# Kernel tuning notes

Hardware: AMD Instinct MI355X
Metric: run time of the kernel (lower is better)

Reference implementation:

```python
import jax, jax.numpy as jnp
import numpy as np
from jax import lax

NUM_ITER = 20


def setup_inputs() -> dict:
    key = jax.random.key(0)
    k1, k2, k3, k4 = jax.random.split(key, 4)
    B, C, H, W = 4, 16, 384, 384
    z_k = jax.random.normal(k1, (B, 2, H, W), dtype=jnp.float32)
    x0 = jax.random.normal(k2, (B, 2, H, W), dtype=jnp.float32)
    csm = jax.random.normal(k3, (B, 2, C, H, W), dtype=jnp.float32)
    mask = jax.random.randint(k4, (B, H, W), 0, 2, dtype=jnp.int32)
    lam = jnp.asarray([0.05], dtype=jnp.float32)  # nn.Parameter init value
    return {"z_k": z_k, "x0": x0, "csm": csm, "lam": lam, "mask": mask}


def _r2c(x):
    # [.., 2, ...] real at axis 1 -> complex
    return lax.complex(x[:, 0], x[:, 1])


def reference(z_k, x0, csm, lam, mask):
    zc = _r2c(z_k)          # [B,H,W] complex64
    b = _r2c(x0)            # [B,H,W] complex64
    coil = _r2c(csm)        # [B,C,H,W] complex64
    m = mask.astype(jnp.float32)  # [B,H,W] binary sampling mask
    lam_s = lam[0]

    def A_fwd(x):           # image [B,H,W] -> masked coil k-space [B,C,H,W]
        return m[:, None] * jnp.fft.fft2(coil * x[:, None])

    def A_adj(k):           # coil k-space [B,C,H,W] -> image [B,H,W]
        return jnp.sum(jnp.conj(coil) * jnp.fft.ifft2(m[:, None] * k), axis=1)

    L = 1.0

    def body(i, carry):
        x, y, t = carry
        grad = A_adj(A_fwd(y) - b[:, None])
        xn = y - (1.0 / L) * grad
        xn = xn - lam_s * (xn - zc)
        # complex prox: clamp real and imag parts at 0
        xn = lax.complex(jnp.maximum(xn.real, 0.0), jnp.maximum(xn.imag, 0.0))
        tn = (1.0 + jnp.sqrt(1.0 + 4.0 * t * t)) / 2.0
        yn = xn + (t - 1.0) / tn * (xn - x)
        return xn, yn, tn

    x_init = jnp.zeros_like(b)
    x, y, t = lax.fori_loop(0, NUM_ITER, body,
                            (x_init, x_init, jnp.float32(1.0)))
    # c2r along axis=1
    return jnp.stack([x.real, x.imag], axis=1)
```

## Files before the change

kernel.cpp:

```cpp
#include <hip/hip_runtime.h>
#include <math.h>


#define NN 384
#define BB 4
#define CC 16
#define NITER 20
#define LNPAD 432
#define PI_F 3.14159265358979323846f
#define TWOPI_F 6.28318530717958647692f

__device__ __forceinline__ int LID(int i) { return i + (i >> 3); }

__device__ __forceinline__ float2 cmulf(float2 a, float2 b) {
  return make_float2(a.x * b.x - a.y * b.y, a.x * b.y + a.y * b.x);
}

template<int CTRL>
__device__ __forceinline__ float dppx(float v) {
  int s = __float_as_int(v);
  return __int_as_float(__builtin_amdgcn_update_dpp(s, s, CTRL, 0xF, 0xF, true));
}

template<int H>
__device__ __forceinline__ float2 exch(float2 v) {
  if constexpr (H == 1) {
    return make_float2(dppx<0xB1>(v.x), dppx<0xB1>(v.y));
  } else if constexpr (H == 2) {
    return make_float2(dppx<0x4E>(v.x), dppx<0x4E>(v.y));
  } else if constexpr (H == 8) {
    return make_float2(dppx<0x128>(v.x), dppx<0x128>(v.y));
  } else {
    return make_float2(__shfl_xor(v.x, H), __shfl_xor(v.y, H));
  }
}

template<int DIR>
__device__ __forceinline__ void dft4(float2* v) {
  float ax = v[0].x + v[2].x, ay = v[0].y + v[2].y;
  float bx = v[0].x - v[2].x, by = v[0].y - v[2].y;
  float cx = v[1].x + v[3].x, cy = v[1].y + v[3].y;
  float dx = v[1].x - v[3].x, dy = v[1].y - v[3].y;
  float dix, diy;
  if (DIR < 0) { dix = dy; diy = -dx; }
  else         { dix = -dy; diy = dx; }
  v[0] = make_float2(ax + cx, ay + cy);
  v[2] = make_float2(ax - cx, ay - cy);
  v[1] = make_float2(bx + dix, by + diy);
  v[3] = make_float2(bx - dix, by - diy);
}

template<int SIGN>
__device__ __forceinline__ void dft3(float2 a, float2 b, float2 c,
                                     float2& X0, float2& X1, float2& X2) {
  const float S3 = 0.86602540378443864676f;
  float ux = b.x + c.x, uy = b.y + c.y;
  float dx = b.x - c.x, dy = b.y - c.y;
  float mx = a.x - 0.5f * ux, my = a.y - 0.5f * uy;
  float ex = S3 * dx, ey = S3 * dy;
  X0 = make_float2(a.x + ux, a.y + uy);
  if (SIGN < 0) {
    X1 = make_float2(mx + ey, my - ex);
    X2 = make_float2(mx - ey, my + ex);
  } else {
    X1 = make_float2(mx - ey, my + ex);
    X2 = make_float2(mx + ey, my - ex);
  }
}

template<int SIGN>
__device__ __forceinline__ void dft6(float2* v) {
  const float S3 = 0.86602540378443864676f;
  float2 E0, E1, E2, O0, O1, O2;
  dft3<SIGN>(v[0], v[2], v[4], E0, E1, E2);
  dft3<SIGN>(v[1], v[3], v[5], O0, O1, O2);
  const float ss = (SIGN < 0) ? -S3 : S3;
  float2 T1 = cmulf(O1, make_float2(0.5f, ss));
  float2 T2 = cmulf(O2, make_float2(-0.5f, ss));
  v[0] = make_float2(E0.x + O0.x, E0.y + O0.y);
  v[1] = make_float2(E1.x + T1.x, E1.y + T1.y);
  v[2] = make_float2(E2.x + T2.x, E2.y + T2.y);
  v[3] = make_float2(E0.x - O0.x, E0.y - O0.y);
  v[4] = make_float2(E1.x - T1.x, E1.y - T1.y);
  v[5] = make_float2(E2.x - T2.x, E2.y - T2.y);
}


template<int H>
__device__ __forceinline__ void dif_step1(float2 v[6], float s, float csl, float snl) {
#pragma unroll
  for (int r = 0; r < 6; ++r) {
    float2 o = exch<H>(v[r]);
    float dx = fmaf(s, v[r].x, o.x);
    float dy = fmaf(s, v[r].y, o.y);
    v[r] = make_float2(dx * csl - dy * snl, dx * snl + dy * csl);
  }
}
template<int H>
__device__ __forceinline__ void dif_step1_notw(float2 v[6], float s) {
#pragma unroll
  for (int r = 0; r < 6; ++r) {
    float2 o = exch<H>(v[r]);
    v[r] = make_float2(fmaf(s, v[r].x, o.x), fmaf(s, v[r].y, o.y));
  }
}
template<int H>
__device__ __forceinline__ void dif_step2(float2 u[6], float2 v[6],
                                          float s, float csl, float snl) {
#pragma unroll
  for (int r = 0; r < 6; ++r) {
    float2 ou = exch<H>(u[r]);
    float2 ov = exch<H>(v[r]);
    float dux = fmaf(s, u[r].x, ou.x), duy = fmaf(s, u[r].y, ou.y);
    float dvx = fmaf(s, v[r].x, ov.x), dvy = fmaf(s, v[r].y, ov.y);
    u[r] = make_float2(dux * csl - duy * snl, dux * snl + duy * csl);
    v[r] = make_float2(dvx * csl - dvy * snl, dvx * snl + dvy * csl);
  }
}
template<int H>
__device__ __forceinline__ void dif_step2_notw(float2 u[6], float2 v[6], float s) {
#pragma unroll
  for (int r = 0; r < 6; ++r) {
    float2 ou = exch<H>(u[r]);
    float2 ov = exch<H>(v[r]);
    u[r] = make_float2(fmaf(s, u[r].x, ou.x), fmaf(s, u[r].y, ou.y));
    v[r] = make_float2(fmaf(s, v[r].x, ov.x), fmaf(s, v[r].y, ov.y));
  }
}

template<int H>
__device__ __forceinline__ void dit_step2(float2 u[6], float2 v[6],
                                          float s, float csl, float snl) {
#pragma unroll
  for (int r = 0; r < 6; ++r) {
    float2 bu = make_float2(u[r].x * csl - u[r].y * snl, u[r].x * snl + u[r].y * csl);
    float2 bv = make_float2(v[r].x * csl - v[r].y * snl, v[r].x * snl + v[r].y * csl);
    float2 ou = exch<H>(bu);
    float2 ov = exch<H>(bv);
    u[r] = make_float2(fmaf(s, bu.x, ou.x), fmaf(s, bu.y, ou.y));
    v[r] = make_float2(fmaf(s, bv.x, ov.x), fmaf(s, bv.y, ov.y));
  }
}
template<int H>
__device__ __forceinline__ void dit_step2_notw(float2 u[6], float2 v[6], float s) {
#pragma unroll
  for (int r = 0; r < 6; ++r) {
    float2 ou = exch<H>(u[r]);
    float2 ov = exch<H>(v[r]);
    u[r] = make_float2(fmaf(s, u[r].x, ou.x), fmaf(s, u[r].y, ou.y));
    v[r] = make_float2(fmaf(s, v[r].x, ov.x), fmaf(s, v[r].y, ov.y));
  }
}

template<int SIGN>
__device__ __forceinline__ void dif64t(float2 v[6], int t, float tc, float tss) {
  { int j = t & 31; bool hi = (t & 32) != 0;
    float cs = __shfl(tc, j), sn = __shfl(tss, j);
    float s = hi ? -1.f : 1.f, csl = hi ? cs : 1.f, snl = hi ? sn : 0.f;
    dif_step1<32>(v, s, csl, snl); }
  { int j = (t & 15) << 1; bool hi = (t & 16) != 0;
    float cs = __shfl(tc, j), sn = __shfl(tss, j);
    float s = hi ? -1.f : 1.f, csl = hi ? cs : 1.f, snl = hi ? sn : 0.f;
    dif_step1<16>(v, s, csl, snl); }
  { int j = (t & 7) << 2; bool hi = (t & 8) != 0;
    float cs = __shfl(tc, j), sn = __shfl(tss, j);
    float s = hi ? -1.f : 1.f, csl = hi ? cs : 1.f, snl = hi ? sn : 0.f;
    dif_step1<8>(v, s, csl, snl); }
  { int j = (t & 3) << 3; bool hi = (t & 4) != 0;
    float cs = __shfl(tc, j), sn = __shfl(tss, j);
    float s = hi ? -1.f : 1.f, csl = hi ? cs : 1.f, snl = hi ? sn : 0.f;
    dif_step1<4>(v, s, csl, snl); }
  { bool hi = (t & 2) != 0, iq = (t & 1) != 0;
    float s = hi ? -1.f : 1.f;
    float c2 = (hi && iq) ? 0.f : 1.f;
    float s2 = (hi && iq) ? (float)SIGN : 0.f;
    dif_step1<2>(v, s, c2, s2); }
  { bool hi = (t & 1) != 0;
    float s = hi ? -1.f : 1.f;
    dif_step1_notw<1>(v, s); }
}

template<int SIGN>
__device__ __forceinline__ void dif64t2(float2 u[6], float2 v[6], int t,
                                        float tc, float tss) {
  { int j = t & 31; bool hi = (t & 32) != 0;
    float cs = __shfl(tc, j), sn = __shfl(tss, j);
    float s = hi ? -1.f : 1.f, csl = hi ? cs : 1.f, snl = hi ? sn : 0.f;
    dif_step2<32>(u, v, s, csl, snl); }
  { int j = (t & 15) << 1; bool hi = (t & 16) != 0;
    float cs = __shfl(tc, j), sn = __shfl(tss, j);
    float s = hi ? -1.f : 1.f, csl = hi ? cs : 1.f, snl = hi ? sn : 0.f;
    dif_step2<16>(u, v, s, csl, snl); }
  { int j = (t & 7) << 2; bool hi = (t & 8) != 0;
    float cs = __shfl(tc, j), sn = __shfl(tss, j);
    float s = hi ? -1.f : 1.f, csl = hi ? cs : 1.f, snl = hi ? sn : 0.f;
    dif_step2<8>(u, v, s, csl, snl); }
  { int j = (t & 3) << 3; bool hi = (t & 4) != 0;
    float cs = __shfl(tc, j), sn = __shfl(tss, j);
    float s = hi ? -1.f : 1.f, csl = hi ? cs : 1.f, snl = hi ? sn : 0.f;
    dif_step2<4>(u, v, s, csl, snl); }
  { bool hi = (t & 2) != 0, iq = (t & 1) != 0;
    float s = hi ? -1.f : 1.f;
    float c2 = (hi && iq) ? 0.f : 1.f;
    float s2 = (hi && iq) ? (float)SIGN : 0.f;
    dif_step2<2>(u, v, s, c2, s2); }
  { bool hi = (t & 1) != 0;
    float s = hi ? -1.f : 1.f;
    dif_step2_notw<1>(u, v, s); }
}

template<int SIGN>
__device__ __forceinline__ void dit64t2(float2 u[6], float2 v[6], int t,
                                        float tc, float tss) {
  { bool hi = (t & 1) != 0;
    float s = hi ? -1.f : 1.f;
    dit_step2_notw<1>(u, v, s); }
  { bool hi = (t & 2) != 0, iq = (t & 1) != 0;
    float s = hi ? -1.f : 1.f;
    float c2 = (hi && iq) ? 0.f : 1.f;
    float s2 = (hi && iq) ? (float)SIGN : 0.f;
    dit_step2<2>(u, v, s, c2, s2); }
  { int j = (t & 3) << 3; bool hi = (t & 4) != 0;
    float cs = __shfl(tc, j), sn = __shfl(tss, j);
    float s = hi ? -1.f : 1.f, csl = hi ? cs : 1.f, snl = hi ? sn : 0.f;
    dit_step2<4>(u, v, s, csl, snl); }
  { int j = (t & 7) << 2; bool hi = (t & 8) != 0;
    float cs = __shfl(tc, j), sn = __shfl(tss, j);
    float s = hi ? -1.f : 1.f, csl = hi ? cs : 1.f, snl = hi ? sn : 0.f;
    dit_step2<8>(u, v, s, csl, snl); }
  { int j = (t & 15) << 1; bool hi = (t & 16) != 0;
    float cs = __shfl(tc, j), sn = __shfl(tss, j);
    float s = hi ? -1.f : 1.f, csl = hi ? cs : 1.f, snl = hi ? sn : 0.f;
    dit_step2<16>(u, v, s, csl, snl); }
  { int j = t & 31; bool hi = (t & 32) != 0;
    float cs = __shfl(tc, j), sn = __shfl(tss, j);
    float s = hi ? -1.f : 1.f, csl = hi ? cs : 1.f, snl = hi ? sn : 0.f;
    dit_step2<32>(u, v, s, csl, snl); }
}

template<int SIGN>
__device__ __forceinline__ void fwd384t(float2 v[6], int t, float tc, float tss,
                                        const float2 w[5]) {
  dft6<SIGN>(v);
#pragma unroll
  for (int r = 1; r < 6; ++r) v[r] = cmulf(v[r], w[r - 1]);
  dif64t<SIGN>(v, t, tc, tss);
}

template<int SIGN>
__device__ __forceinline__ void fwd384t2(float2 u[6], float2 v[6], int t,
                                         float tc, float tss, const float2 w[5]) {
  dft6<SIGN>(u);
  dft6<SIGN>(v);
#pragma unroll
  for (int r = 1; r < 6; ++r) { u[r] = cmulf(u[r], w[r - 1]); v[r] = cmulf(v[r], w[r - 1]); }
  dif64t2<SIGN>(u, v, t, tc, tss);
}

template<int SIGN>
__device__ __forceinline__ void bwd384t2(float2 u[6], float2 v[6], int t,
                                         float tc, float tss, const float2 w[5],
                                         float sc0) {
  dit64t2<SIGN>(u, v, t, tc, tss);
  u[0].x *= sc0; u[0].y *= sc0;
  v[0].x *= sc0; v[0].y *= sc0;
#pragma unroll
  for (int r = 1; r < 6; ++r) { u[r] = cmulf(u[r], w[r - 1]); v[r] = cmulf(v[r], w[r - 1]); }
  dft6<SIGN>(u);
  dft6<SIGN>(v);
}

template<int R, int NS, int DIR>
__device__ __forceinline__ void fft_stage(const float2* S, float2* D, int t) {
  constexpr int NR = NN / R;
#pragma unroll
  for (int rep = 0; rep < (NR + 63) / 64; ++rep) {
    int j = t + rep * 64;
    if (j < NR) {
      float2 v[R];
#pragma unroll
      for (int r = 0; r < R; ++r) v[r] = S[LID(j + r * NR)];
      if constexpr (NS > 1) {
        float ang = (float)DIR * (TWOPI_F / (float)(NS * R)) * (float)(j % NS);
        float sv, cv;
        __sincosf(ang, &sv, &cv);
        float2 w = make_float2(cv, sv);
        float2 wr = w;
#pragma unroll
        for (int r = 1; r < R; ++r) { v[r] = cmulf(v[r], wr); wr = cmulf(wr, w); }
      }
      if constexpr (R == 4) dft4<DIR>(v); else dft6<DIR>(v);
      int base = (j / NS) * (NS * R) + (j % NS);
#pragma unroll
      for (int r = 0; r < R; ++r) D[LID(base + r * NS)] = v[r];
    }
  }
}

template<int DIR>
__device__ __forceinline__ void fft384(float2* A, float2* Bf, int t) {
  fft_stage<4, 1,  DIR>(A,  Bf, t); __syncthreads();
  fft_stage<4, 4,  DIR>(Bf, A,  t); __syncthreads();
  fft_stage<4, 16, DIR>(A,  Bf, t); __syncthreads();
  fft_stage<6, 64, DIR>(Bf, A,  t); __syncthreads();
}

__global__ __launch_bounds__(256) void k_e(const float2* __restrict__ czb,
                                           float2* __restrict__ xbuf,
                                           float2* __restrict__ ybuf) {
  long i = (long)blockIdx.x * 256 + threadIdx.x;
  float2 cz = czb[i];
  float2 x = make_float2(fmaxf(cz.x, 0.f), fmaxf(cz.y, 0.f));
  xbuf[i] = x;
  ybuf[i] = x;
}

__global__ __launch_bounds__(256) void k_p1(const float2* __restrict__ ybuf,
                                            const float* __restrict__ csm,
                                            float2* __restrict__ W1) {
  int t = threadIdx.x & 63;
  int w = threadIdx.x >> 6;
  long gl = (long)blockIdx.x * 4 + w;
  int y = (int)(gl % NN);
  long bc = gl / NN;
  long b = bc >> 4, c = bc & 15;
  long rowoff = (long)y * NN;
  float tc, ts; __sincosf((float)(t & 31) * (PI_F / 32.0f), &ts, &tc);
  float tsf = -ts;
  float2 w0; __sincosf(-(float)t * (TWOPI_F / 384.0f), &w0.y, &w0.x);
  float2 wf[5];
  wf[0] = w0;
#pragma unroll
  for (int r = 1; r < 5; ++r) wf[r] = cmulf(wf[r - 1], w0);
  const float2* yrow = ybuf + b * (long)(NN * NN) + rowoff;
  const float* crow_re = csm + (b * 2 * CC + c) * (long)(NN * NN) + rowoff;
  const float* crow_im = crow_re + (long)CC * NN * NN;
  float2 v[6];
#pragma unroll
  for (int k = 0; k < 6; ++k) {
    int x = t + 64 * k;
    float2 yv = yrow[x];
    float cre = crow_re[x], cim = crow_im[x];
    v[k] = make_float2(yv.x * cre - yv.y * cim, yv.x * cim + yv.y * cre);
  }
  fwd384t<-1>(v, t, tc, tsf, wf);
  float2* orow = W1 + gl * NN;
#pragma unroll
  for (int r = 0; r < 6; ++r) orow[t + 64 * r] = v[r];
}

#define P2PAD 392
__global__ __launch_bounds__(256) void k_p2(float2* __restrict__ W1,
                                            const unsigned char* __restrict__ maskPT) {
  __shared__ float ldsR[8][P2PAD];
  __shared__ float ldsI[8][P2PAD];
  int tid = threadIdx.x;
  const int nwg = BB * CC * (NN / 8);
  int l = ((int)blockIdx.x & 7) * (nwg >> 3) + ((int)blockIdx.x >> 3);
  int xt = l % (NN / 8);
  long bc = l / (NN / 8);
  long b = bc >> 4;
  int s0 = xt * 8;
  long sbase = bc * (long)(NN * NN);
  int w = tid >> 6, t = tid & 63;
  float tc, ts; __sincosf((float)(t & 31) * (PI_F / 32.0f), &ts, &tc);
  float tsf = -ts;
  float2 w0; __sincosf(-(float)t * (TWOPI_F / 384.0f), &w0.y, &w0.x);
  float2 wf[5], wb[5];
  wf[0] = w0;
#pragma unroll
  for (int r = 1; r < 5; ++r) wf[r] = cmulf(wf[r - 1], w0);
  const float inv = 1.0f / NN;
#pragma unroll
  for (int r = 0; r < 5; ++r) wb[r] = make_float2(wf[r].x * inv, -wf[r].y * inv);
  const float4* W1v = (const float4*)W1;
  long f4base = (sbase >> 1) + (s0 >> 1);
#pragma unroll
  for (int k = 0; k < 6; ++k) {
    int e = tid + k * 256; int y = e >> 2; int q = e & 3;
    float4 val = W1v[f4base + (long)y * (NN / 2) + q];
    ldsR[2 * q][y] = val.x; ldsI[2 * q][y] = val.y;
    ldsR[2 * q + 1][y] = val.z; ldsI[2 * q + 1][y] = val.w;
  }
  __syncthreads();
  const unsigned char* mb = maskPT + b * (long)(NN * NN);
  {
    int c0 = 2 * w, c1 = 2 * w + 1;
    float2 u[6], v[6];
#pragma unroll
    for (int k = 0; k < 6; ++k) {
      u[k] = make_float2(ldsR[c0][t + 64 * k], ldsI[c0][t + 64 * k]);
      v[k] = make_float2(ldsR[c1][t + 64 * k], ldsI[c1][t + 64 * k]);
    }
    fwd384t2<-1>(u, v, t, tc, tsf, wf);
    const unsigned char* m0 = mb + (long)(s0 + c0) * NN;
    const unsigned char* m1 = mb + (long)(s0 + c1) * NN;
#pragma unroll
    for (int r = 0; r < 6; ++r) {
      float mv0 = (float)m0[t + 64 * r];
      float mv1 = (float)m1[t + 64 * r];
      u[r].x *= mv0; u[r].y *= mv0;
      v[r].x *= mv1; v[r].y *= mv1;
    }
    bwd384t2<1>(u, v, t, tc, ts, wb, inv);
#pragma unroll
    for (int k = 0; k < 6; ++k) {
      ldsR[c0][t + 64 * k] = u[k].x;
      ldsI[c0][t + 64 * k] = u[k].y;
      ldsR[c1][t + 64 * k] = v[k].x;
      ldsI[c1][t + 64 * k] = v[k].y;
    }
  }
  __syncthreads();
  float4* W1o = (float4*)W1;
#pragma unroll
  for (int k = 0; k < 6; ++k) {
    int e = tid + k * 256; int y = e >> 2; int q = e & 3;
    float4 val;
    val.x = ldsR[2 * q][y]; val.y = ldsI[2 * q][y];
    val.z = ldsR[2 * q + 1][y]; val.w = ldsI[2 * q + 1][y];
    W1o[f4base + (long)y * (NN / 2) + q] = val;
  }
}

__global__ __launch_bounds__(256) void k_p3(const float2* __restrict__ W1,
                                            const float* __restrict__ csm,
                                            const float2* __restrict__ czb,
                                            const float* __restrict__ lamp,
                                            float2* __restrict__ xbuf,
                                            float2* __restrict__ ybuf,
                                            float* __restrict__ outp,
                                            float beta, int last) {
  __shared__ float2 part[4][NN];
  int tid = threadIdx.x;
  int w = tid >> 6, t = tid & 63;
  long gl = blockIdx.x;
  long b = gl / NN;
  int y = (int)(gl % NN);
  long rowoff = (long)y * NN;
  float tc, ts; __sincosf((float)(t & 31) * (PI_F / 32.0f), &ts, &tc);
  float2 w0; __sincosf((float)t * (TWOPI_F / 384.0f), &w0.y, &w0.x);
  float2 wb[5];
  wb[0] = w0;
#pragma unroll
  for (int r = 1; r < 5; ++r) wb[r] = cmulf(wb[r - 1], w0);
  float2 acc[6];
#pragma unroll
  for (int k = 0; k < 6; ++k) acc[k] = make_float2(0.f, 0.f);
#pragma unroll
  for (int ci = 0; ci < 4; ci += 2) {
    int c0 = w * 4 + ci, c1 = c0 + 1;
    const float2* row0 = W1 + ((b * CC + c0) * (long)NN + y) * NN;
    const float2* row1 = W1 + ((b * CC + c1) * (long)NN + y) * NN;
    float2 u[6], v[6];
#pragma unroll
    for (int r = 0; r < 6; ++r) { u[r] = row0[t + 64 * r]; v[r] = row1[t + 64 * r]; }
    bwd384t2<1>(u, v, t, tc, ts, wb, 1.0f);
    const float* cre0 = csm + (b * 2 * CC + c0) * (long)(NN * NN) + rowoff;
    const float* cim0 = cre0 + (long)CC * NN * NN;
    const float* cre1 = csm + (b * 2 * CC + c1) * (long)(NN * NN) + rowoff;
    const float* cim1 = cre1 + (long)CC * NN * NN;
#pragma unroll
    for (int k = 0; k < 6; ++k) {
      int x = t + 64 * k;
      float a0 = cre0[x], b0 = cim0[x];
      float a1 = cre1[x], b1 = cim1[x];
      acc[k].x += (a0 * u[k].x + b0 * u[k].y) + (a1 * v[k].x + b1 * v[k].y);
      acc[k].y += (a0 * u[k].y - b0 * u[k].x) + (a1 * v[k].y - b1 * v[k].x);
    }
  }
#pragma unroll
  for (int k = 0; k < 6; ++k) part[w][t + 64 * k] = acc[k];
  __syncthreads();
  float lamv = lamp[0];
  float oml = 1.0f - lamv;
  long pbase = b * (long)(NN * NN) + rowoff;
  for (int e = tid; e < NN; e += 256) {
    float Qx = (part[0][e].x + part[1][e].x + part[2][e].x + part[3][e].x) * (1.0f / NN);
    float Qy = (part[0][e].y + part[1][e].y + part[2][e].y + part[3][e].y) * (1.0f / NN);
    float2 yv = ybuf[pbase + e];
    float2 cz = czb[pbase + e];
    float xr = oml * (yv.x - Qx) + cz.x;
    float xi = oml * (yv.y - Qy) + cz.y;
    xr = fmaxf(xr, 0.f);
    xi = fmaxf(xi, 0.f);
    if (last) {
      outp[(b * 2 + 0) * (long)(NN * NN) + rowoff + e] = xr;
      outp[(b * 2 + 1) * (long)(NN * NN) + rowoff + e] = xi;
    } else {
      float2 xo = xbuf[pbase + e];
      xbuf[pbase + e] = make_float2(xr, xi);
      ybuf[pbase + e] = make_float2(xr + beta * (xr - xo.x), xi + beta * (xi - xo.y));
    }
  }
}

__global__ __launch_bounds__(256) void k_mpre(const int* __restrict__ mask,
                                              unsigned char* __restrict__ maskPT) {
  long i = (long)blockIdx.x * 256 + threadIdx.x;
  long b = i / (NN * NN);
  int rem = (int)(i % (NN * NN));
  int sx = rem / NN, sy = rem % NN;
  int fx = (sx >> 6) + 6 * (int)(__brev((unsigned)(sx & 63)) >> 26);
  int fy = (sy >> 6) + 6 * (int)(__brev((unsigned)(sy & 63)) >> 26);
  maskPT[i] = (unsigned char)mask[b * (long)(NN * NN) + (long)fy * NN + fx];
}

__global__ __launch_bounds__(256) void k_preA(const float* __restrict__ x0,
                                              const int* __restrict__ mask,
                                              float2* __restrict__ T) {
  __shared__ float2 U[4][LNPAD], V[4][LNPAD];
  int tid = threadIdx.x;
  int line = tid >> 6, t = tid & 63;
  long gl0 = (long)blockIdx.x * 4;
#pragma unroll
  for (int k = 0; k < 6; ++k) {
    int e = tid + k * 256; int l = e / NN; int x = e % NN;
    long gl = gl0 + l;
    long b = gl / NN;
    int y = (int)(gl % NN);
    long pidx = (long)y * NN + x;
    float mv = (float)mask[b * (long)(NN * NN) + pidx];
    float br = x0[(b * 2 + 0) * (long)(NN * NN) + pidx] * mv;
    float bi = x0[(b * 2 + 1) * (long)(NN * NN) + pidx] * mv;
    U[l][LID(x)] = make_float2(br, bi);
  }
  __syncthreads();
  fft384<1>(U[line], V[line], t);
#pragma unroll
  for (int k = 0; k < 6; ++k) {
    int e = tid + k * 256; int l = e / NN; int x = e % NN;
    float2 u = U[l][LID(x)];
    T[(gl0 + l) * NN + x] = make_float2(u.x * (1.0f / NN), u.y * (1.0f / NN));
  }
}

__global__ __launch_bounds__(256) void k_preB(const float2* __restrict__ T,
                                              float2* __restrict__ r0) {
  __shared__ float2 tile[NN][17];
  __shared__ float2 U[4][LNPAD], V[4][LNPAD];
  int tid = threadIdx.x;
  int xt = blockIdx.x % (NN / 16);
  long b = blockIdx.x / (NN / 16);
  int x0c = xt * 16;
  long sbase = b * (long)(NN * NN);
#pragma unroll
  for (int k = 0; k < 24; ++k) {
    int e = tid + k * 256; int y = e >> 4; int c = e & 15;
    tile[y][c] = T[sbase + (long)y * NN + x0c + c];
  }
  __syncthreads();
  int line = tid >> 6, t = tid & 63;
  for (int g = 0; g < 4; ++g) {
#pragma unroll
    for (int k = 0; k < 6; ++k) {
      int e = tid + k * 256; int l = e / NN; int y = e % NN;
      U[l][LID(y)] = tile[y][4 * g + l];
    }
    __syncthreads();
    fft384<1>(U[line], V[line], t);
#pragma unroll
    for (int k = 0; k < 6; ++k) {
      int e = tid + k * 256; int l = e / NN; int y = e % NN;
      float2 u = U[l][LID(y)];
      tile[y][4 * g + l] = make_float2(u.x * (1.0f / NN), u.y * (1.0f / NN));
    }
    __syncthreads();
  }
#pragma unroll
  for (int k = 0; k < 24; ++k) {
    int e = tid + k * 256; int y = e >> 4; int c = e & 15;
    r0[sbase + (long)y * NN + x0c + c] = tile[y][c];
  }
}

__global__ __launch_bounds__(256) void k_preC(const float* __restrict__ csm,
                                              const float2* __restrict__ r0,
                                              const float* __restrict__ zk,
                                              const float* __restrict__ lamp,
                                              float2* __restrict__ czb) {
  long i = (long)blockIdx.x * 256 + threadIdx.x;
  long b = i / (NN * NN);
  long p = i % (NN * NN);
  float sr = 0.f, si = 0.f;
#pragma unroll
  for (int c = 0; c < CC; ++c) {
    sr += csm[(b * 2 * CC + c) * (long)(NN * NN) + p];
    si -= csm[((b * 2 + 1) * CC + c) * (long)(NN * NN) + p];
  }
  float2 r = r0[i];
  float cstx = sr * r.x - si * r.y;
  float csty = sr * r.y + si * r.x;
  float lamv = lamp[0];
  float oml = 1.0f - lamv;
  float zr = zk[(b * 2 + 0) * (long)(NN * NN) + p];
  float zi = zk[(b * 2 + 1) * (long)(NN * NN) + p];
  czb[i] = make_float2(oml * cstx + lamv * zr, oml * csty + lamv * zi);
}

extern "C" void kernel_launch(void* const* d_in, const int* in_sizes, int n_in,
                              void* d_out, int out_size, void* d_ws, size_t ws_size,
                              hipStream_t stream) {
  const float* zk  = (const float*)d_in[0];
  const float* x0  = (const float*)d_in[1];
  const float* csm = (const float*)d_in[2];
  const float* lam = (const float*)d_in[3];
  const int*   msk = (const int*)d_in[4];
  float* out = (float*)d_out;

  size_t img = (size_t)BB * NN * NN;
  float2* W1   = (float2*)d_ws;
  float2* ybuf = W1 + (size_t)BB * CC * NN * NN;
  float2* xbuf = ybuf + img;
  float2* czb  = xbuf + img;
  unsigned char* maskPT = (unsigned char*)(czb + img);
  float2* T  = W1;
  float2* r0 = W1 + img;

  double tcur = 1.0;
  float betas[NITER];
  for (int i = 0; i < NITER; ++i) {
    double tn = (1.0 + sqrt(1.0 + 4.0 * tcur * tcur)) * 0.5;
    betas[i] = (float)((tcur - 1.0) / tn);
    tcur = tn;
  }

  k_mpre<<<(BB * NN * NN) / 256, 256, 0, stream>>>(msk, maskPT);
  k_preA<<<BB * NN / 4, 256, 0, stream>>>(x0, msk, T);
  k_preB<<<BB * (NN / 16), 256, 0, stream>>>(T, r0);
  k_preC<<<(BB * NN * NN) / 256, 256, 0, stream>>>(csm, r0, zk, lam, czb);
  k_e<<<(BB * NN * NN) / 256, 256, 0, stream>>>(czb, xbuf, ybuf);
  for (int i = 1; i < NITER; ++i) {
    k_p1<<<BB * CC * NN / 4, 256, 0, stream>>>(ybuf, csm, W1);
    k_p2<<<BB * CC * (NN / 8), 256, 0, stream>>>(W1, maskPT);
    k_p3<<<BB * NN, 256, 0, stream>>>(W1, csm, czb, lam, xbuf, ybuf, out,
                                      betas[i], (i == NITER - 1) ? 1 : 0);
  }
}
```

Before: 1.961 ms.

## Rework k_p2 column FFT as 24x16 decomposition with 16 lanes per column

The k_p2 column-FFT kernel is restructured so each 384-point transform runs on 16 lanes holding 24 points each, using a register-resident radix-24 DFT plus a 16-point shuffle butterfly, instead of 64 lanes with 6 points each. This cuts the number of cross-lane exchange stages and shuffles per transform, and the block shrinks to 128 threads. The mask permutation precompute changes to match the new output ordering, and the mask is read with uchar4 vector loads. Holding 24 complex values per thread raises register pressure and may lower occupancy.

New measurement: 1.885 ms. 3.9% less time.

```diff
diff --git a/kernel.cpp b/kernel.cpp
--- a/kernel.cpp
+++ b/kernel.cpp
@@ -85,71 +85,97 @@
   v[5] = make_float2(E2.x - T2.x, E2.y - T2.y);
 }
 
-
-template<int H>
-__device__ __forceinline__ void dif_step1(float2 v[6], float s, float csl, float snl) {
-#pragma unroll
-  for (int r = 0; r < 6; ++r) {
+__device__ __forceinline__ float2 w24v(int j, int sign) {
+  constexpr float C[16] = {
+    1.f, 0.96592582628906831f, 0.86602540378443865f, 0.70710678118654752f,
+    0.5f, 0.25881904510252076f, 0.f, -0.25881904510252076f,
+    -0.5f, -0.70710678118654752f, -0.86602540378443865f, -0.96592582628906831f,
+    -1.f, -0.96592582628906831f, -0.86602540378443865f, -0.70710678118654752f };
+  constexpr float S[16] = {
+    0.f, 0.25881904510252076f, 0.5f, 0.70710678118654752f,
+    0.86602540378443865f, 0.96592582628906831f, 1.f, 0.96592582628906831f,
+    0.86602540378443865f, 0.70710678118654752f, 0.5f, 0.25881904510252076f,
+    0.f, -0.25881904510252076f, -0.5f, -0.70710678118654752f };
+  return make_float2(C[j], sign < 0 ? -S[j] : S[j]);
+}
+
+template<int SIGN>
+__device__ __forceinline__ void dft24(float2 v[24]) {
+#pragma unroll
+  for (int a = 0; a < 4; ++a) {
+    float2 tmp[6];
+#pragma unroll
+    for (int b = 0; b < 6; ++b) tmp[b] = v[a + 4 * b];
+    dft6<SIGN>(tmp);
+#pragma unroll
+    for (int k6 = 0; k6 < 6; ++k6) v[a + 4 * k6] = tmp[k6];
+  }
+  float2 o[24];
+#pragma unroll
+  for (int k6 = 0; k6 < 6; ++k6) {
+    float2 h[4];
+    h[0] = v[4 * k6];
+#pragma unroll
+    for (int a = 1; a < 4; ++a) {
+      int j = a * k6;
+      h[a] = (j == 0) ? v[a + 4 * k6] : cmulf(v[a + 4 * k6], w24v(j, SIGN));
+    }
+    dft4<SIGN>(h);
+#pragma unroll
+    for (int m = 0; m < 4; ++m) o[k6 + 6 * m] = h[m];
+  }
+#pragma unroll
+  for (int i = 0; i < 24; ++i) v[i] = o[i];
+}
+
+template<int H, int NR>
+__device__ __forceinline__ void dif_stepN(float2* v, float s, float csl, float snl) {
+#pragma unroll
+  for (int r = 0; r < NR; ++r) {
     float2 o = exch<H>(v[r]);
     float dx = fmaf(s, v[r].x, o.x);
     float dy = fmaf(s, v[r].y, o.y);
     v[r] = make_float2(dx * csl - dy * snl, dx * snl + dy * csl);
   }
 }
-template<int H>
-__device__ __forceinline__ void dif_step1_notw(float2 v[6], float s) {
-#pragma unroll
-  for (int r = 0; r < 6; ++r) {
+template<int H, int NR>
+__device__ __forceinline__ void dif_stepN_notw(float2* v, float s) {
+#pragma unroll
+  for (int r = 0; r < NR; ++r) {
     float2 o = exch<H>(v[r]);
     v[r] = make_float2(fmaf(s, v[r].x, o.x), fmaf(s, v[r].y, o.y));
   }
 }
+template<int H, int NR>
+__device__ __forceinline__ void dit_stepN(float2* v, float s, float csl, float snl) {
+#pragma unroll
+  for (int r = 0; r < NR; ++r) {
+    float2 bt = make_float2(v[r].x * csl - v[r].y * snl,
+                            v[r].x * snl + v[r].y * csl);
+    float2 o = exch<H>(bt);
+    v[r] = make_float2(fmaf(s, bt.x, o.x), fmaf(s, bt.y, o.y));
+  }
+}
+template<int H, int NR>
+__device__ __forceinline__ void dit_stepN_notw(float2* v, float s) {
+#pragma unroll
+  for (int r = 0; r < NR; ++r) {
+    float2 o = exch<H>(v[r]);
+    v[r] = make_float2(fmaf(s, v[r].x, o.x), fmaf(s, v[r].y, o.y));
+  }
+}
+
 template<int H>
 __device__ __forceinline__ void dif_step2(float2 u[6], float2 v[6],
                                           float s, float csl, float snl) {
-#pragma unroll
-  for (int r = 0; r < 6; ++r) {
-    float2 ou = exch<H>(u[r]);
-    float2 ov = exch<H>(v[r]);
-    float dux = fmaf(s, u[r].x, ou.x), duy = fmaf(s, u[r].y, ou.y);
-    float dvx = fmaf(s, v[r].x, ov.x), dvy = fmaf(s, v[r].y, ov.y);
-    u[r] = make_float2(dux * csl - duy * snl, dux * snl + duy * csl);
-    v[r] = make_float2(dvx * csl - dvy * snl, dvx * snl + dvy * csl);
-  }
-}
-template<int H>
-__device__ __forceinline__ void dif_step2_notw(float2 u[6], float2 v[6], float s) {
-#pragma unroll
-  for (int r = 0; r < 6; ++r) {
-    float2 ou = exch<H>(u[r]);
-    float2 ov = exch<H>(v[r]);
-    u[r] = make_float2(fmaf(s, u[r].x, ou.x), fmaf(s, u[r].y, ou.y));
-    v[r] = make_float2(fmaf(s, v[r].x, ov.x), fmaf(s, v[r].y, ov.y));
-  }
-}
-
+  dif_stepN<H, 6>(u, s, csl, snl);
+  dif_stepN<H, 6>(v, s, csl, snl);
+}
 template<int H>
 __device__ __forceinline__ void dit_step2(float2 u[6], float2 v[6],
                                           float s, float csl, float snl) {
-#pragma unroll
-  for (int r = 0; r < 6; ++r) {
-    float2 bu = make_float2(u[r].x * csl - u[r].y * snl, u[r].x * snl + u[r].y * csl);
-    float2 bv = make_float2(v[r].x * csl - v[r].y * snl, v[r].x * snl + v[r].y * csl);
-    float2 ou = exch<H>(bu);
-    float2 ov = exch<H>(bv);
-    u[r] = make_float2(fmaf(s, bu.x, ou.x), fmaf(s, bu.y, ou.y));
-    v[r] = make_float2(fmaf(s, bv.x, ov.x), fmaf(s, bv.y, ov.y));
-  }
-}
-template<int H>
-__device__ __forceinline__ void dit_step2_notw(float2 u[6], float2 v[6], float s) {
-#pragma unroll
-  for (int r = 0; r < 6; ++r) {
-    float2 ou = exch<H>(u[r]);
-    float2 ov = exch<H>(v[r]);
-    u[r] = make_float2(fmaf(s, u[r].x, ou.x), fmaf(s, u[r].y, ou.y));
-    v[r] = make_float2(fmaf(s, v[r].x, ov.x), fmaf(s, v[r].y, ov.y));
-  }
+  dit_stepN<H, 6>(u, s, csl, snl);
+  dit_stepN<H, 6>(v, s, csl, snl);
 }
 
 template<int SIGN>
@@ -157,56 +183,26 @@
   { int j = t & 31; bool hi = (t & 32) != 0;
     float cs = __shfl(tc, j), sn = __shfl(tss, j);
     float s = hi ? -1.f : 1.f, csl = hi ? cs : 1.f, snl = hi ? sn : 0.f;
-    dif_step1<32>(v, s, csl, snl); }
+    dif_stepN<32, 6>(v, s, csl, snl); }
   { int j = (t & 15) << 1; bool hi = (t & 16) != 0;
     float cs = __shfl(tc, j), sn = __shfl(tss, j);
     float s = hi ? -1.f : 1.f, csl = hi ? cs : 1.f, snl = hi ? sn : 0.f;
-    dif_step1<16>(v, s, csl, snl); }
+    dif_stepN<16, 6>(v, s, csl, snl); }
   { int j = (t & 7) << 2; bool hi = (t & 8) != 0;
     float cs = __shfl(tc, j), sn = __shfl(tss, j);
     float s = hi ? -1.f : 1.f, csl = hi ? cs : 1.f, snl = hi ? sn : 0.f;
-    dif_step1<8>(v, s, csl, snl); }
+    dif_stepN<8, 6>(v, s, csl, snl); }
   { int j = (t & 3) << 3; bool hi = (t & 4) != 0;
     float cs = __shfl(tc, j), sn = __shfl(tss, j);
     float s = hi ? -1.f : 1.f, csl = hi ? cs : 1.f, snl = hi ? sn : 0.f;
-    dif_step1<4>(v, s, csl, snl); }
+    dif_stepN<4, 6>(v, s, csl, snl); }
   { bool hi = (t & 2) != 0, iq = (t & 1) != 0;
     float s = hi ? -1.f : 1.f;
     float c2 = (hi && iq) ? 0.f : 1.f;
     float s2 = (hi && iq) ? (float)SIGN : 0.f;
-    dif_step1<2>(v, s, c2, s2); }
+    dif_stepN<2, 6>(v, s, c2, s2); }
   { bool hi = (t & 1) != 0;
-    float s = hi ? -1.f : 1.f;
-    dif_step1_notw<1>(v, s); }
-}
-
-template<int SIGN>
-__device__ __forceinline__ void dif64t2(float2 u[6], float2 v[6], int t,
-                                        float tc, float tss) {
-  { int j = t & 31; bool hi = (t & 32) != 0;
-    float cs = __shfl(tc, j), sn = __shfl(tss, j);
-    float s = hi ? -1.f : 1.f, csl = hi ? cs : 1.f, snl = hi ? sn : 0.f;
-    dif_step2<32>(u, v, s, csl, snl); }
-  { int j = (t & 15) << 1; bool hi = (t & 16) != 0;
-    float cs = __shfl(tc, j), sn = __shfl(tss, j);
-    float s = hi ? -1.f : 1.f, csl = hi ? cs : 1.f, snl = hi ? sn : 0.f;
-    dif_step2<16>(u, v, s, csl, snl); }
-  { int j = (t & 7) << 2; bool hi = (t & 8) != 0;
-    float cs = __shfl(tc, j), sn = __shfl(tss, j);
-    float s = hi ? -1.f : 1.f, csl = hi ? cs : 1.f, snl = hi ? sn : 0.f;
-    dif_step2<8>(u, v, s, csl, snl); }
-  { int j = (t & 3) << 3; bool hi = (t & 4) != 0;
-    float cs = __shfl(tc, j), sn = __shfl(tss, j);
-    float s = hi ? -1.f : 1.f, csl = hi ? cs : 1.f, snl = hi ? sn : 0.f;
-    dif_step2<4>(u, v, s, csl, snl); }
-  { bool hi = (t & 2) != 0, iq = (t & 1) != 0;
-    float s = hi ? -1.f : 1.f;
-    float c2 = (hi && iq) ? 0.f : 1.f;
-    float s2 = (hi && iq) ? (float)SIGN : 0.f;
-    dif_step2<2>(u, v, s, c2, s2); }
-  { bool hi = (t & 1) != 0;
-    float s = hi ? -1.f : 1.f;
-    dif_step2_notw<1>(u, v, s); }
+    dif_stepN_notw<1, 6>(v, hi ? -1.f : 1.f); }
 }
 
 template<int SIGN>
@@ -214,7 +210,7 @@
                                         float tc, float tss) {
   { bool hi = (t & 1) != 0;
     float s = hi ? -1.f : 1.f;
-    dit_step2_notw<1>(u, v, s); }
+    dit_stepN_notw<1, 6>(u, s); dit_stepN_notw<1, 6>(v, s); }
   { bool hi = (t & 2) != 0, iq = (t & 1) != 0;
     float s = hi ? -1.f : 1.f;
     float c2 = (hi && iq) ? 0.f : 1.f;
@@ -248,16 +244,6 @@
 }
 
 template<int SIGN>
-__device__ __forceinline__ void fwd384t2(float2 u[6], float2 v[6], int t,
-                                         float tc, float tss, const float2 w[5]) {
-  dft6<SIGN>(u);
-  dft6<SIGN>(v);
-#pragma unroll
-  for (int r = 1; r < 6; ++r) { u[r] = cmulf(u[r], w[r - 1]); v[r] = cmulf(v[r], w[r - 1]); }
-  dif64t2<SIGN>(u, v, t, tc, tss);
-}
-
-template<int SIGN>
 __device__ __forceinline__ void bwd384t2(float2 u[6], float2 v[6], int t,
                                          float tc, float tss, const float2 w[5],
                                          float sc0) {
@@ -268,6 +254,76 @@
   for (int r = 1; r < 6; ++r) { u[r] = cmulf(u[r], w[r - 1]); v[r] = cmulf(v[r], w[r - 1]); }
   dft6<SIGN>(u);
   dft6<SIGN>(v);
+}
+
+template<int SIGN>
+__device__ __forceinline__ void dif16x24(float2 v[24], int t, float tc, float tss) {
+  { int j = (t & 7) << 2; bool hi = (t & 8) != 0;
+    float cs = __shfl(tc, j), sn = __shfl(tss, j);
+    float s = hi ? -1.f : 1.f, csl = hi ? cs : 1.f, snl = hi ? sn : 0.f;
+    dif_stepN<8, 24>(v, s, csl, snl); }
+  { int j = (t & 3) << 3; bool hi = (t & 4) != 0;
+    float cs = __shfl(tc, j), sn = __shfl(tss, j);
+    float s = hi ? -1.f : 1.f, csl = hi ? cs : 1.f, snl = hi ? sn : 0.f;
+    dif_stepN<4, 24>(v, s, csl, snl); }
+  { bool hi = (t & 2) != 0, iq = (t & 1) != 0;
+    float s = hi ? -1.f : 1.f;
+    float c2 = (hi && iq) ? 0.f : 1.f;
+    float s2 = (hi && iq) ? (float)SIGN : 0.f;
+    dif_stepN<2, 24>(v, s, c2, s2); }
+  { bool hi = (t & 1) != 0;
+    dif_stepN_notw<1, 24>(v, hi ? -1.f : 1.f); }
+}
+
+template<int SIGN>
+__device__ __forceinline__ void dit16x24(float2 v[24], int t, float tc, float tss) {
+  { bool hi = (t & 1) != 0;
+    dit_stepN_notw<1, 24>(v, hi ? -1.f : 1.f); }
+  { bool hi = (t & 2) != 0, iq = (t & 1) != 0;
+    float s = hi ? -1.f : 1.f;
+    float c2 = (hi && iq) ? 0.f : 1.f;
+    float s2 = (hi && iq) ? (float)SIGN : 0.f;
+    dit_stepN<2, 24>(v, s, c2, s2); }
+  { int j = (t & 3) << 3; bool hi = (t & 4) != 0;
+    float cs = __shfl(tc, j), sn = __shfl(tss, j);
+    float s = hi ? -1.f : 1.f, csl = hi ? cs : 1.f, snl = hi ? sn : 0.f;
+    dit_stepN<4, 24>(v, s, csl, snl); }
+  { int j = (t & 7) << 2; bool hi = (t & 8) != 0;
+    float cs = __shfl(tc, j), sn = __shfl(tss, j);
+    float s = hi ? -1.f : 1.f, csl = hi ? cs : 1.f, snl = hi ? sn : 0.f;
+    dit_stepN<8, 24>(v, s, csl, snl); }
+}
+
+template<int SIGN>
+__device__ __forceinline__ void fwd384q(float2 v[24], int t16, float tc, float tss,
+                                        const float2 Q[6], const float2 P[4]) {
+  dft24<SIGN>(v);
+#pragma unroll
+  for (int k1 = 1; k1 < 24; ++k1) {
+    int m = k1 / 6, q = k1 % 6;
+    float2 x = v[k1];
+    if (q) x = cmulf(x, Q[q]);
+    if (m) x = cmulf(x, P[m]);
+    v[k1] = x;
+  }
+  dif16x24<SIGN>(v, t16, tc, tss);
+}
+
+template<int SIGN>
+__device__ __forceinline__ void bwd384q(float2 v[24], int t16, float tc, float tss,
+                                        const float2 Q[6], const float2 P[4],
+                                        float inv) {
+  dit16x24<SIGN>(v, t16, tc, tss);
+#pragma unroll
+  for (int k1 = 0; k1 < 24; ++k1) {
+    int m = k1 / 6, q = k1 % 6;
+    float2 x = v[k1];
+    if (q) x = cmulf(x, Q[q]);
+    if (m) x = cmulf(x, P[m]);
+    else   x = make_float2(x.x * inv, x.y * inv);
+    v[k1] = x;
+  }
+  dft24<SIGN>(v);
 }
 
 template<int R, int NS, int DIR>
@@ -350,7 +406,7 @@
 }
 
 #define P2PAD 392
-__global__ __launch_bounds__(256) void k_p2(float2* __restrict__ W1,
+__global__ __launch_bounds__(128) void k_p2(float2* __restrict__ W1,
                                             const unsigned char* __restrict__ maskPT) {
   __shared__ float ldsR[8][P2PAD];
   __shared__ float ldsI[8][P2PAD];
@@ -362,60 +418,67 @@
   long b = bc >> 4;
   int s0 = xt * 8;
   long sbase = bc * (long)(NN * NN);
-  int w = tid >> 6, t = tid & 63;
-  float tc, ts; __sincosf((float)(t & 31) * (PI_F / 32.0f), &ts, &tc);
+  int g = tid >> 4, t16 = tid & 15;
+  int tl = tid & 63;
+  float tc, ts; __sincosf((float)(tl & 31) * (PI_F / 32.0f), &ts, &tc);
   float tsf = -ts;
-  float2 w0; __sincosf(-(float)t * (TWOPI_F / 384.0f), &w0.y, &w0.x);
-  float2 wf[5], wb[5];
-  wf[0] = w0;
-#pragma unroll
-  for (int r = 1; r < 5; ++r) wf[r] = cmulf(wf[r - 1], w0);
+  float2 w0; __sincosf(-(float)t16 * (TWOPI_F / 384.0f), &w0.y, &w0.x);
+  float2 q2 = cmulf(w0, w0);
+  float2 q3 = cmulf(q2, w0);
+  float2 q4 = cmulf(q2, q2);
+  float2 q5 = cmulf(q3, q2);
+  float2 p1v = cmulf(q3, q3);
+  float2 p2v = cmulf(p1v, p1v);
+  float2 p3v = cmulf(p2v, p1v);
+  float2 Qf[6] = { make_float2(1.f, 0.f), w0, q2, q3, q4, q5 };
+  float2 Pf[4] = { make_float2(1.f, 0.f), p1v, p2v, p3v };
   const float inv = 1.0f / NN;
-#pragma unroll
-  for (int r = 0; r < 5; ++r) wb[r] = make_float2(wf[r].x * inv, -wf[r].y * inv);
+  float2 Qb[6], Pb[4];
+  Qb[0] = make_float2(1.f, 0.f);
+#pragma unroll
+  for (int i = 1; i < 6; ++i) Qb[i] = make_float2(Qf[i].x, -Qf[i].y);
+  Pb[0] = make_float2(inv, 0.f);
+#pragma unroll
+  for (int m = 1; m < 4; ++m) Pb[m] = make_float2(Pf[m].x * inv, -Pf[m].y * inv);
   const float4* W1v = (const float4*)W1;
   long f4base = (sbase >> 1) + (s0 >> 1);
 #pragma unroll
-  for (int k = 0; k < 6; ++k) {
-    int e = tid + k * 256; int y = e >> 2; int q = e & 3;
+  for (int k = 0; k < 12; ++k) {
+    int e = tid + k * 128; int y = e >> 2; int q = e & 3;
     float4 val = W1v[f4base + (long)y * (NN / 2) + q];
     ldsR[2 * q][y] = val.x; ldsI[2 * q][y] = val.y;
     ldsR[2 * q + 1][y] = val.z; ldsI[2 * q + 1][y] = val.w;
   }
   __syncthreads();
-  const unsigned char* mb = maskPT + b * (long)(NN * NN);
   {
-    int c0 = 2 * w, c1 = 2 * w + 1;
-    float2 u[6], v[6];
-#pragma unroll
-    for (int k = 0; k < 6; ++k) {
-      u[k] = make_float2(ldsR[c0][t + 64 * k], ldsI[c0][t + 64 * k]);
-      v[k] = make_float2(ldsR[c1][t + 64 * k], ldsI[c1][t + 64 * k]);
+    float2 v[24];
+#pragma unroll
+    for (int r = 0; r < 24; ++r)
+      v[r] = make_float2(ldsR[g][t16 + 16 * r], ldsI[g][t16 + 16 * r]);
+    fwd384q<-1>(v, t16, tc, tsf, Qf, Pf);
+    int brt = (int)(__brev((unsigned)t16) >> 28);
+    const unsigned char* mcol =
+        maskPT + b * (long)(NN * NN) + (long)(s0 + g) * NN + 24 * brt;
+#pragma unroll
+    for (int i = 0; i < 6; ++i) {
+      uchar4 mv = ((const uchar4*)mcol)[i];
+      v[4 * i + 0].x *= (float)mv.x; v[4 * i + 0].y *= (float)mv.x;
+      v[4 * i + 1].x *= (float)mv.y; v[4 * i + 1].y *= (float)mv.y;
+      v[4 * i + 2].x *= (float)mv.z; v[4 * i + 2].y *= (float)mv.z;
+      v[4 * i + 3].x *= (float)mv.w; v[4 * i + 3].y *= (float)mv.w;
     }
-    fwd384t2<-1>(u, v, t, tc, tsf, wf);
-    const unsigned char* m0 = mb + (long)(s0 + c0) * NN;
-    const unsigned char* m1 = mb + (long)(s0 + c1) * NN;
-#pragma unroll
-    for (int r = 0; r < 6; ++r) {
-      float mv0 = (float)m0[t + 64 * r];
-      float mv1 = (float)m1[t + 64 * r];
-      u[r].x *= mv0; u[r].y *= mv0;
-      v[r].x *= mv1; v[r].y *= mv1;
-    }
-    bwd384t2<1>(u, v, t, tc, ts, wb, inv);
-#pragma unroll
-    for (int k = 0; k < 6; ++k) {
-      ldsR[c0][t + 64 * k] = u[k].x;
-      ldsI[c0][t + 64 * k] = u[k].y;
-      ldsR[c1][t + 64 * k] = v[k].x;
-      ldsI[c1][t + 64 * k] = v[k].y;
+    bwd384q<1>(v, t16, tc, ts, Qb, Pb, inv);
+#pragma unroll
+    for (int r = 0; r < 24; ++r) {
+      ldsR[g][t16 + 16 * r] = v[r].x;
+      ldsI[g][t16 + 16 * r] = v[r].y;
     }
   }
   __syncthreads();
   float4* W1o = (float4*)W1;
 #pragma unroll
-  for (int k = 0; k < 6; ++k) {
-    int e = tid + k * 256; int y = e >> 2; int q = e & 3;
+  for (int k = 0; k < 12; ++k) {
+    int e = tid + k * 128; int y = e >> 2; int q = e & 3;
     float4 val;
     val.x = ldsR[2 * q][y]; val.y = ldsI[2 * q][y];
     val.z = ldsR[2 * q + 1][y]; val.w = ldsI[2 * q + 1][y];
@@ -500,10 +563,9 @@
   long i = (long)blockIdx.x * 256 + threadIdx.x;
   long b = i / (NN * NN);
   int rem = (int)(i % (NN * NN));
-  int sx = rem / NN, sy = rem % NN;
+  int sx = rem / NN, y = rem % NN;
   int fx = (sx >> 6) + 6 * (int)(__brev((unsigned)(sx & 63)) >> 26);
-  int fy = (sy >> 6) + 6 * (int)(__brev((unsigned)(sy & 63)) >> 26);
-  maskPT[i] = (unsigned char)mask[b * (long)(NN * NN) + (long)fy * NN + fx];
+  maskPT[i] = (unsigned char)mask[b * (long)(NN * NN) + (long)y * NN + fx];
 }
 
 __global__ __launch_bounds__(256) void k_preA(const float* __restrict__ x0,
@@ -632,7 +694,7 @@
   k_e<<<(BB * NN * NN) / 256, 256, 0, stream>>>(czb, xbuf, ybuf);
   for (int i = 1; i < NITER; ++i) {
     k_p1<<<BB * CC * NN / 4, 256, 0, stream>>>(ybuf, csm, W1);
-    k_p2<<<BB * CC * (NN / 8), 256, 0, stream>>>(W1, maskPT);
+    k_p2<<<BB * CC * (NN / 8), 128, 0, stream>>>(W1, maskPT);
     k_p3<<<BB * NN, 256, 0, stream>>>(W1, csm, czb, lam, xbuf, ybuf, out,
                                       betas[i], (i == NITER - 1) ? 1 : 0);
   }
```
